# Kernel tuning notes

Hardware: AMD Instinct MI355X
Metric: run time of the kernel (lower is better)

The kernel has to match this reference:

```python
import jax, jax.numpy as jnp
import numpy as np

HEADS = 4
HEAD_DIM = 32  # hidden_dim // num_heads = 128 // 4
HIDDEN = 128
NEG_SLOPE = 0.2  # GATConv default


def gat_conv(x, src, dst, W, att_src, att_dst, bias):
    """PyG GATConv (concat=True, default negative_slope=0.2), eval mode.
    x: [N, F_in], src/dst: [E] (self-loops already included)."""
    N = x.shape[0]
    h = (x @ W).reshape(N, HEADS, HEAD_DIM)               # [N, H, D]
    a_src = jnp.einsum('nhd,hd->nh', h, att_src)          # [N, H]
    a_dst = jnp.einsum('nhd,hd->nh', h, att_dst)
    e = jax.nn.leaky_relu(a_src[src] + a_dst[dst], NEG_SLOPE)  # [E, H]
    # numerically stable softmax over incoming edges of each dst node
    m = jax.ops.segment_max(e, dst, num_segments=N)
    m = jnp.where(jnp.isfinite(m), m, 0.0)
    p = jnp.exp(e - m[dst])
    denom = jax.ops.segment_sum(p, dst, num_segments=N)
    alpha = p / (denom[dst] + 1e-16)                      # [E, H]
    out = jax.ops.segment_sum(h[src] * alpha[..., None], dst, num_segments=N)
    return out.reshape(N, HEADS * HEAD_DIM) + bias


def setup_inputs() -> dict:
    key = jax.random.key(0)
    ks = jax.random.split(key, 20)
    n_news, n_tweets, E = 20000, 80000, 1600000
    N = n_news + n_tweets
    s = 0.05
    inp = {
        'x_news': jax.random.normal(ks[0], (n_news, 768), jnp.float32),
        'x_tweets': jax.random.normal(ks[1], (n_tweets, 512), jnp.float32),
        'edge_index': jax.random.randint(ks[2], (2, E), 0, N, jnp.int32),
        'W_news': jax.random.normal(ks[3], (768, HIDDEN), jnp.float32) * s,
        'b_news': jnp.zeros((HIDDEN,), jnp.float32),
        'W_tw': jax.random.normal(ks[4], (512, HIDDEN), jnp.float32) * s,
        'b_tw': jnp.zeros((HIDDEN,), jnp.float32),
        'gat1_W': jax.random.normal(ks[5], (HIDDEN, HIDDEN), jnp.float32) * s,
        'gat1_as': jax.random.normal(ks[6], (HEADS, HEAD_DIM), jnp.float32) * s,
        'gat1_ad': jax.random.normal(ks[7], (HEADS, HEAD_DIM), jnp.float32) * s,
        'gat1_b': jnp.zeros((HIDDEN,), jnp.float32),
        'gat2_W': jax.random.normal(ks[8], (HIDDEN, HIDDEN), jnp.float32) * s,
        'gat2_as': jax.random.normal(ks[9], (HEADS, HEAD_DIM), jnp.float32) * s,
        'gat2_ad': jax.random.normal(ks[10], (HEADS, HEAD_DIM), jnp.float32) * s,
        'gat2_b': jnp.zeros((HIDDEN,), jnp.float32),
        'Wc1': jax.random.normal(ks[11], (HIDDEN, HIDDEN // 2), jnp.float32) * s,
        'bc1': jnp.zeros((HIDDEN // 2,), jnp.float32),
        'Wc2': jax.random.normal(ks[12], (HIDDEN // 2, 2), jnp.float32) * s,
        'bc2': jnp.zeros((2,), jnp.float32),
    }
    return inp


def reference(x_news, x_tweets, edge_index, W_news, b_news, W_tw, b_tw,
              gat1_W, gat1_as, gat1_ad, gat1_b,
              gat2_W, gat2_as, gat2_ad, gat2_b,
              Wc1, bc1, Wc2, bc2):
    n_news = x_news.shape[0]
    # encoders (dropout is identity in eval)
    h_news = jax.nn.relu(x_news @ W_news + b_news)
    h_tw = jax.nn.relu(x_tweets @ W_tw + b_tw)
    x = jnp.concatenate([h_news, h_tw], axis=0)           # [N, 128]
    N = x.shape[0]
    # GATConv default: add self-loops
    loops = jnp.arange(N, dtype=edge_index.dtype)
    src = jnp.concatenate([edge_index[0], loops])
    dst = jnp.concatenate([edge_index[1], loops])
    x = jax.nn.elu(gat_conv(x, src, dst, gat1_W, gat1_as, gat1_ad, gat1_b))
    x = jax.nn.elu(gat_conv(x, src, dst, gat2_W, gat2_as, gat2_ad, gat2_b))
    news_emb = x[:n_news]
    out = jax.nn.relu(news_emb @ Wc1 + bc1) @ Wc2 + bc2   # [n_news, 2]
    return out
```

## Files before the change

### kernel.cpp

```cpp
#include <hip/hip_runtime.h>
#include <hip/hip_bf16.h>
#include <type_traits>

typedef __attribute__((ext_vector_type(8))) short bf16x8;
typedef __attribute__((ext_vector_type(8))) unsigned short u16x8;
typedef __attribute__((ext_vector_type(4))) float f32x4;

__device__ __forceinline__ unsigned short f2b(float f) {
  union { float f; unsigned u; } c; c.f = f;
  return (unsigned short)((c.u + 0x7fffu + ((c.u >> 16) & 1u)) >> 16);
}
__device__ __forceinline__ float b2f(unsigned short v) {
  return __uint_as_float((unsigned)v << 16);
}

constexpr int BK = 64;
constexpr int LS = BK + 8;

template<int BM, int K, int ACT, int LOGITS, typename AT>
__device__ __forceinline__ void gemm_body(
    int bid, unsigned short* As,
    const AT* __restrict__ A, int M,
    const unsigned short* __restrict__ WT, const float* __restrict__ bias,
    unsigned short* __restrict__ C,
    const float* __restrict__ att_src, const float* __restrict__ att_dst,
    float* __restrict__ a_src, float* __restrict__ a_dst)
{
  constexpr int WTM = BM;
  constexpr int WTN = 32;
  constexpr int MF = WTM / 16;
  constexpr int NF = WTN / 16;
  constexpr int HPW = 1;
  const int t = threadIdx.x;
  const int lane = t & 63;
  const int wc = t >> 6;
  const long row0 = (long)bid * BM;

  f32x4 acc[MF][NF] = {};

  for (int k0 = 0; k0 < K; k0 += BK) {
    if constexpr (std::is_same<AT, float>::value) {
#pragma unroll
      for (int i = 0; i < BM / 16; ++i) {
        int idx = t + i * 256;
        int r = idx >> 4;
        int kq = idx & 15;
        long gr = row0 + r; if (gr >= M) gr = M - 1;
        const float4 v = *(const float4*)(A + gr * K + k0 + kq * 4);
        ushort4 b;
        b.x = f2b(v.x); b.y = f2b(v.y); b.z = f2b(v.z); b.w = f2b(v.w);
        *(ushort4*)(&As[r * LS + kq * 4]) = b;
      }
    } else {
#pragma unroll
      for (int i = 0; i < BM / 32; ++i) {
        int idx = t + i * 256;
        int r = idx >> 3;
        int k8 = idx & 7;
        long gr = row0 + r; if (gr >= M) gr = M - 1;
        u16x8 v = *(const u16x8*)(A + gr * K + k0 + k8 * 8);
        *(u16x8*)(&As[r * LS + k8 * 8]) = v;
      }
    }
    __syncthreads();
#pragma unroll
    for (int kk = 0; kk < BK; kk += 32) {
      const int koff = kk + (lane >> 4) * 8;
      bf16x8 af[MF], bfr[NF];
#pragma unroll
      for (int n = 0; n < NF; ++n)
        bfr[n] = *(const bf16x8*)(WT + (long)(wc * WTN + n * 16 + (lane & 15)) * K + k0 + koff);
#pragma unroll
      for (int m = 0; m < MF; ++m)
        af[m] = *(const bf16x8*)(&As[(m * 16 + (lane & 15)) * LS + koff]);
#pragma unroll
      for (int m = 0; m < MF; ++m)
#pragma unroll
        for (int n = 0; n < NF; ++n)
          acc[m][n] = __builtin_amdgcn_mfma_f32_16x16x32_bf16(af[m], bfr[n], acc[m][n], 0, 0, 0);
    }
    __syncthreads();
  }

  float asv[NF], adv[NF];
  if (LOGITS) {
#pragma unroll
    for (int n = 0; n < NF; ++n) {
      int dim = n * 16 + (lane & 15);
      asv[n] = att_src[wc * 32 + dim];
      adv[n] = att_dst[wc * 32 + dim];
    }
  }

#pragma unroll
  for (int m = 0; m < MF; ++m) {
#pragma unroll
    for (int j = 0; j < 4; ++j) {
      long gr = row0 + m * 16 + (lane >> 4) * 4 + j;
      if (gr < M) {
#pragma unroll
        for (int n = 0; n < NF; ++n) {
          int c = wc * WTN + n * 16 + (lane & 15);
          float v = acc[m][n][j];
          if (bias) v += bias[c];
          if (ACT == 1) v = fmaxf(v, 0.f);
          C[gr * 128 + c] = f2b(v);
        }
      }
      if (LOGITS) {
        float sa = fmaf(acc[m][0][j], asv[0], acc[m][1][j] * asv[1]);
        float da = fmaf(acc[m][0][j], adv[0], acc[m][1][j] * adv[1]);
#pragma unroll
        for (int off = 1; off < 16; off <<= 1) {
          sa += __shfl_xor(sa, off);
          da += __shfl_xor(da, off);
        }
        if ((lane & 15) == 0 && gr < M) {
          a_src[gr * 4 + wc] = sa;
          a_dst[gr * 4 + wc] = da;
        }
      }
    }
  }
}

__device__ __forceinline__ void hist_body(int bid, int* cnt, const int* __restrict__ dst,
                                          int E, int* __restrict__ bcount, int nb)
{
  int t = threadIdx.x;
  for (int b = t; b < 512; b += 256) cnt[b] = 0;
  __syncthreads();
  int e0 = bid * 8192;
  for (int i = 0; i < 32; ++i) {
    int e = e0 + i * 256 + t;
    if (e < E) atomicAdd(&cnt[dst[e] >> 8], 1);
  }
  __syncthreads();
  for (int b = t; b < nb; b += 256) {
    int c = cnt[b];
    if (c > 0) atomicAdd(&bcount[b], c);
  }
}

__device__ __forceinline__ void scatter_body(int bid, int* s, const int* __restrict__ src,
                                             const int* __restrict__ dst, int E,
                                             int* __restrict__ bcur, int2* __restrict__ pairs)
{
  int* cnt = s;
  int* base = s + 512;
  int* rcur = s + 1024;
  int t = threadIdx.x;
  for (int b = t; b < 512; b += 256) { cnt[b] = 0; rcur[b] = 0; }
  __syncthreads();
  int e0 = bid * 8192;
  for (int i = 0; i < 32; ++i) {
    int e = e0 + i * 256 + t;
    if (e < E) atomicAdd(&cnt[dst[e] >> 8], 1);
  }
  __syncthreads();
  for (int b = t; b < 512; b += 256) {
    int c = cnt[b];
    if (c > 0) base[b] = atomicAdd(&bcur[b], c);
  }
  __syncthreads();
  for (int i = 0; i < 32; ++i) {
    int e = e0 + i * 256 + t;
    if (e < E) {
      int d = dst[e];
      int b = d >> 8;
      int off = atomicAdd(&rcur[b], 1);
      int2 p; p.x = src[e]; p.y = d;
      pairs[base[b] + off] = p;
    }
  }
}

__global__ __launch_bounds__(256) void mega1_kernel(
    int nb_tw, int nb_news,
    const float* __restrict__ x_tw, int n_tw, const unsigned short* __restrict__ WT_tw,
    const float* __restrict__ b_tw, unsigned short* __restrict__ out_tw,
    const float* __restrict__ x_news, int n_news, const unsigned short* __restrict__ WT_news,
    const float* __restrict__ b_news, unsigned short* __restrict__ out_news,
    const int* __restrict__ dst, int E, int* __restrict__ bcount, int nb)
{
  __shared__ unsigned short sh[64 * LS];
  int bid = blockIdx.x;
  if (bid < nb_tw) {
    gemm_body<64, 512, 1, 0, float>(bid, sh, x_tw, n_tw, WT_tw, b_tw, out_tw,
                                    nullptr, nullptr, nullptr, nullptr);
  } else if (bid < nb_tw + nb_news) {
    gemm_body<32, 768, 1, 0, float>(bid - nb_tw, sh, x_news, n_news, WT_news,
                                    b_news, out_news, nullptr, nullptr, nullptr, nullptr);
  } else {
    hist_body(bid - nb_tw - nb_news, (int*)sh, dst, E, bcount, nb);
  }
}

__global__ __launch_bounds__(256) void mega3_kernel(
    int nb_gemm,
    const unsigned short* __restrict__ x_feat, int N, const unsigned short* __restrict__ WT_g1,
    unsigned short* __restrict__ h_feat,
    const float* __restrict__ g1as, const float* __restrict__ g1ad,
    float* __restrict__ a_src, float* __restrict__ a_dst,
    const int* __restrict__ src, const int* __restrict__ dst, int E,
    int* __restrict__ bcur, int2* __restrict__ pairs)
{
  __shared__ unsigned short sh[64 * LS];
  int bid = blockIdx.x;
  if (bid < nb_gemm) {
    gemm_body<64, 128, 0, 1, unsigned short>(bid, sh, x_feat, N, WT_g1, nullptr,
                                             h_feat, g1as, g1ad, a_src, a_dst);
  } else {
    scatter_body(bid - nb_gemm, (int*)sh, src, dst, E, bcur, pairs);
  }
}

template<int BM, int K, int ACT, int LOGITS, typename AT>
__global__ __launch_bounds__(256) void gemm_kernel(
    const AT* __restrict__ A, int M,
    const unsigned short* __restrict__ WT, const float* __restrict__ bias,
    unsigned short* __restrict__ C,
    const float* __restrict__ att_src, const float* __restrict__ att_dst,
    float* __restrict__ a_src, float* __restrict__ a_dst)
{
  __shared__ unsigned short sh[BM * LS];
  gemm_body<BM, K, ACT, LOGITS, AT>(blockIdx.x, sh, A, M, WT, bias, C,
                                    att_src, att_dst, a_src, a_dst);
}

__global__ void transpose_all_kernel(const float* __restrict__ W0, unsigned short* __restrict__ T0,
                                     const float* __restrict__ W1, unsigned short* __restrict__ T1,
                                     const float* __restrict__ W2, unsigned short* __restrict__ T2,
                                     const float* __restrict__ W3, unsigned short* __restrict__ T3)
{
  int r = blockIdx.x * 256 + threadIdx.x;
  if (r < 128 * 768) { int c = r / 768, k = r - c * 768; T0[r] = f2b(W0[(size_t)k * 128 + c]); return; }
  r -= 128 * 768;
  if (r < 128 * 512) { int c = r / 512, k = r - c * 512; T1[r] = f2b(W1[(size_t)k * 128 + c]); return; }
  r -= 128 * 512;
  if (r < 128 * 128) { T2[r] = f2b(W2[(size_t)(r & 127) * 128 + (r >> 7)]); return; }
  r -= 128 * 128;
  if (r < 128 * 128) { T3[r] = f2b(W3[(size_t)(r & 127) * 128 + (r >> 7)]); return; }
}

__global__ __launch_bounds__(512) void bucket_scan_kernel(const int* __restrict__ bcount, int nb, int E,
                                                          int* __restrict__ bstart, int* __restrict__ bcur,
                                                          int* __restrict__ row_ptr, int N)
{
  __shared__ int s[512];
  int t = threadIdx.x;
  int my = (t < nb) ? bcount[t] : 0;
  s[t] = my;
  __syncthreads();
  for (int off = 1; off < 512; off <<= 1) {
    int v = (t >= off) ? s[t - off] : 0;
    __syncthreads();
    s[t] += v;
    __syncthreads();
  }
  int excl = s[t] - my;
  if (t < nb) { bstart[t] = excl; bcur[t] = excl; }
  if (t == 0) { bstart[nb] = E; row_ptr[N] = E; }
}

__global__ __launch_bounds__(256) void bucket_csr_kernel(const int2* __restrict__ pairs,
                                                         const int* __restrict__ bstart, int N,
                                                         int* __restrict__ row_ptr, int* __restrict__ col_idx)
{
  __shared__ int cnt[256];
  __shared__ int excl[256];
  __shared__ int cur[256];
  int t = threadIdx.x;
  int nodebase = blockIdx.x << 8;
  int start = bstart[blockIdx.x];
  int size = bstart[blockIdx.x + 1] - start;
  cnt[t] = 0;
  __syncthreads();
  for (int i = t; i < size; i += 256)
    atomicAdd(&cnt[pairs[start + i].y & 255], 1);
  __syncthreads();
  int my = cnt[t];
  excl[t] = my;
  __syncthreads();
  for (int off = 1; off < 256; off <<= 1) {
    int v = (t >= off) ? excl[t - off] : 0;
    __syncthreads();
    excl[t] += v;
    __syncthreads();
  }
  int ex = excl[t] - my;
  if (nodebase + t < N) row_ptr[nodebase + t] = start + ex;
  excl[t] = ex;
  cur[t] = 0;
  __syncthreads();
  for (int i = t; i < size; i += 256) {
    int2 p = pairs[start + i];
    int local = p.y & 255;
    int pos = start + excl[local] + atomicAdd(&cur[local], 1);
    col_idx[pos] = p.x;
  }
}

__global__ void gat_aggregate_kernel(const unsigned short* __restrict__ h, const float* __restrict__ a_src,
                                     const float* __restrict__ a_dst, const int* __restrict__ row_ptr,
                                     const int* __restrict__ col_idx, const float* __restrict__ bias,
                                     int N, unsigned short* __restrict__ out)
{
  int n = (blockIdx.x * blockDim.x + threadIdx.x) >> 6;
  int lane = threadIdx.x & 63;
  if (n >= N) return;
  const int sub = lane >> 4;
  const int sl = lane & 15;
  const int head = sl >> 2;
  const int beg = row_ptr[n], end = row_ptr[n + 1];
  const float adst = a_dst[(size_t)n * 4 + head];

  float slf = a_src[(size_t)n * 4 + head] + adst;
  slf = fmaxf(slf, 0.2f * slf);
  float ps = (sub == 0) ? __expf(slf) : 0.f;
  float denom = ps;
  float acc[8];
  {
    const u16x8 hs = *(const u16x8*)(h + (size_t)n * 128 + 8 * sl);
#pragma unroll
    for (int j = 0; j < 8; ++j) acc[j] = ps * b2f(hs[j]);
  }

  int e = beg + sub;
  for (; e + 4 < end; e += 8) {
    const int s0 = col_idx[e];
    const int s1 = col_idx[e + 4];
    const u16x8 h0 = *(const u16x8*)(h + (size_t)s0 * 128 + 8 * sl);
    const u16x8 h1 = *(const u16x8*)(h + (size_t)s1 * 128 + 8 * sl);
    float l0 = a_src[(size_t)s0 * 4 + head] + adst;
    float l1 = a_src[(size_t)s1 * 4 + head] + adst;
    l0 = fmaxf(l0, 0.2f * l0);
    l1 = fmaxf(l1, 0.2f * l1);
    const float p0 = __expf(l0);
    const float p1 = __expf(l1);
    denom += p0 + p1;
#pragma unroll
    for (int j = 0; j < 8; ++j) {
      acc[j] = fmaf(p0, b2f(h0[j]), acc[j]);
      acc[j] = fmaf(p1, b2f(h1[j]), acc[j]);
    }
  }
  if (e < end) {
    const int s = col_idx[e];
    const u16x8 hv = *(const u16x8*)(h + (size_t)s * 128 + 8 * sl);
    float lg = a_src[(size_t)s * 4 + head] + adst;
    lg = fmaxf(lg, 0.2f * lg);
    const float p = __expf(lg);
    denom += p;
#pragma unroll
    for (int j = 0; j < 8; ++j) acc[j] = fmaf(p, b2f(hv[j]), acc[j]);
  }

#pragma unroll
  for (int j = 0; j < 8; ++j) {
    acc[j] += __shfl_xor(acc[j], 16);
    acc[j] += __shfl_xor(acc[j], 32);
  }
  denom += __shfl_xor(denom, 16);
  denom += __shfl_xor(denom, 32);

  if (sub == 0) {
    const float inv = 1.0f / (denom + 1e-16f);
    const float4 b0 = *(const float4*)(bias + 8 * sl);
    const float4 b1 = *(const float4*)(bias + 8 * sl + 4);
    float o[8];
    o[0] = acc[0] * inv + b0.x; o[1] = acc[1] * inv + b0.y;
    o[2] = acc[2] * inv + b0.z; o[3] = acc[3] * inv + b0.w;
    o[4] = acc[4] * inv + b1.x; o[5] = acc[5] * inv + b1.y;
    o[6] = acc[6] * inv + b1.z; o[7] = acc[7] * inv + b1.w;
    u16x8 r;
#pragma unroll
    for (int j = 0; j < 8; ++j) {
      float v = (o[j] > 0.f) ? o[j] : expm1f(o[j]);
      r[j] = f2b(v);
    }
    *(u16x8*)(out + (size_t)n * 128 + 8 * sl) = r;
  }
}

__global__ void classifier_kernel(const unsigned short* __restrict__ x, const float* __restrict__ Wc1,
                                  const float* __restrict__ bc1, const float* __restrict__ Wc2,
                                  const float* __restrict__ bc2, float* __restrict__ out, int M)
{
  int row = (blockIdx.x * blockDim.x + threadIdx.x) >> 6;
  int lane = threadIdx.x & 63;
  if (row >= M) return;
  const unsigned short* xr = x + (size_t)row * 128;
  float c = 0.f;
#pragma unroll 8
  for (int k = 0; k < 128; k += 2) {
    unsigned v = *(const unsigned*)(xr + k);
    c = fmaf(__uint_as_float(v << 16), Wc1[k * 64 + lane], c);
    c = fmaf(__uint_as_float(v & 0xffff0000u), Wc1[(k + 1) * 64 + lane], c);
  }
  c += bc1[lane];
  c = fmaxf(c, 0.f);
  float o0 = c * Wc2[lane * 2 + 0];
  float o1 = c * Wc2[lane * 2 + 1];
#pragma unroll
  for (int off = 1; off < 64; off <<= 1) {
    o0 += __shfl_xor(o0, off);
    o1 += __shfl_xor(o1, off);
  }
  if (lane == 0) {
    out[(size_t)row * 2 + 0] = o0 + bc2[0];
    out[(size_t)row * 2 + 1] = o1 + bc2[1];
  }
}

extern "C" void kernel_launch(void* const* d_in, const int* in_sizes, int n_in,
                              void* d_out, int out_size, void* d_ws, size_t ws_size,
                              hipStream_t stream)
{
  const float* x_news = (const float*)d_in[0];
  const float* x_tw   = (const float*)d_in[1];
  const int*   ei     = (const int*)d_in[2];
  const float* W_news = (const float*)d_in[3];
  const float* b_news = (const float*)d_in[4];
  const float* W_tw   = (const float*)d_in[5];
  const float* b_tw   = (const float*)d_in[6];
  const float* g1W  = (const float*)d_in[7];
  const float* g1as = (const float*)d_in[8];
  const float* g1ad = (const float*)d_in[9];
  const float* g1b  = (const float*)d_in[10];
  const float* g2W  = (const float*)d_in[11];
  const float* g2as = (const float*)d_in[12];
  const float* g2ad = (const float*)d_in[13];
  const float* g2b  = (const float*)d_in[14];
  const float* Wc1  = (const float*)d_in[15];
  const float* bc1  = (const float*)d_in[16];
  const float* Wc2  = (const float*)d_in[17];
  const float* bc2  = (const float*)d_in[18];

  const int n_news = in_sizes[0] / 768;
  const int n_tw   = in_sizes[1] / 512;
  const int N = n_news + n_tw;
  const int E = in_sizes[2] / 2;
  const int* src = ei;
  const int* dst = ei + E;
  const int nb = (N + 255) >> 8;

  char* ws = (char*)d_ws;
  size_t off = 0;
  auto alloc = [&](size_t bytes) -> void* {
    void* p = ws + off;
    off += (bytes + 255) & ~(size_t)255;
    return p;
  };
  unsigned short* x_feat = (unsigned short*)alloc((size_t)N * 128 * 2);
  unsigned short* h_feat = (unsigned short*)alloc((size_t)N * 128 * 2);
  float* a_src   = (float*)alloc((size_t)N * 4 * 4);
  float* a_dst   = (float*)alloc((size_t)N * 4 * 4);
  int*   row_ptr = (int*)alloc((size_t)(N + 1) * 4);
  int*   col_idx = (int*)alloc((size_t)E * 4);
  int2*  pairs   = (int2*)alloc((size_t)E * 8);
  int*   bcount  = (int*)alloc(2048);
  int*   bstart  = (int*)alloc(2052);
  int*   bcur    = (int*)alloc(2048);
  unsigned short* WT_news = (unsigned short*)alloc((size_t)128 * 768 * 2);
  unsigned short* WT_tw   = (unsigned short*)alloc((size_t)128 * 512 * 2);
  unsigned short* WT_g1   = (unsigned short*)alloc((size_t)128 * 128 * 2);
  unsigned short* WT_g2   = (unsigned short*)alloc((size_t)128 * 128 * 2);

  hipMemsetAsync(bcount, 0, 2048, stream);

  transpose_all_kernel<<<768, 256, 0, stream>>>(W_news, WT_news, W_tw, WT_tw, g1W, WT_g1, g2W, WT_g2);

  const int nb_tw = (n_tw + 63) / 64;
  const int nb_news = (n_news + 31) / 32;
  const int nb_hist = (E + 8191) / 8192;
  mega1_kernel<<<nb_tw + nb_news + nb_hist, 256, 0, stream>>>(
      nb_tw, nb_news,
      x_tw, n_tw, WT_tw, b_tw, x_feat + (size_t)n_news * 128,
      x_news, n_news, WT_news, b_news, x_feat,
      dst, E, bcount, nb);

  bucket_scan_kernel<<<1, 512, 0, stream>>>(bcount, nb, E, bstart, bcur, row_ptr, N);

  const int nb_g = (N + 63) / 64;
  mega3_kernel<<<nb_g + nb_hist, 256, 0, stream>>>(
      nb_g, x_feat, N, WT_g1, h_feat, g1as, g1ad, a_src, a_dst,
      src, dst, E, bcur, pairs);

  bucket_csr_kernel<<<nb, 256, 0, stream>>>(pairs, bstart, N, row_ptr, col_idx);

  gat_aggregate_kernel<<<(N + 3) / 4, 256, 0, stream>>>(h_feat, a_src, a_dst, row_ptr, col_idx, g1b, N, x_feat);

  gemm_kernel<64, 128, 0, 1, unsigned short><<<nb_g, 256, 0, stream>>>(
      x_feat, N, WT_g2, nullptr, h_feat, g2as, g2ad, a_src, a_dst);
  gat_aggregate_kernel<<<(N + 3) / 4, 256, 0, stream>>>(h_feat, a_src, a_dst, row_ptr, col_idx, g2b, N, x_feat);

  classifier_kernel<<<(n_news + 3) / 4, 256, 0, stream>>>(x_feat, Wc1, bc1, Wc2, bc2, (float*)d_out, n_news);
}
```

Measured before the change: 375.0 us.

## Double-buffer GEMM A tiles in LDS with register prefetch of next K slice

The GEMM body now loads the next K slice of A into registers while MFMAs run on the current LDS buffer, then writes it to a second LDS buffer, removing one barrier per iteration. The goal is to hide global load latency behind compute in the encoder and GAT projection GEMMs. It doubles the LDS footprint and adds register pressure, which can reduce occupancy. It also grows LDS for the fused histogram and scatter blocks that share the same kernels.

Measured after the change: 378.3 us. No clear change (+0.9%).

```diff
diff --git a/kernel.cpp b/kernel.cpp
--- a/kernel.cpp
+++ b/kernel.cpp
@@ -26,43 +26,67 @@
     const float* __restrict__ att_src, const float* __restrict__ att_dst,
     float* __restrict__ a_src, float* __restrict__ a_dst)
 {
-  constexpr int WTM = BM;
+  constexpr bool F32 = std::is_same<AT, float>::value;
   constexpr int WTN = 32;
-  constexpr int MF = WTM / 16;
-  constexpr int NF = WTN / 16;
-  constexpr int HPW = 1;
+  constexpr int MF = BM / 16;
+  constexpr int NF = 2;
+  constexpr int NLD = F32 ? (BM / 16) : (BM / 32);
   const int t = threadIdx.x;
   const int lane = t & 63;
   const int wc = t >> 6;
   const long row0 = (long)bid * BM;
 
   f32x4 acc[MF][NF] = {};
-
-  for (int k0 = 0; k0 < K; k0 += BK) {
-    if constexpr (std::is_same<AT, float>::value) {
-#pragma unroll
-      for (int i = 0; i < BM / 16; ++i) {
+  float4 rF[F32 ? NLD : 1];
+  u16x8  rB[F32 ? 1 : NLD];
+
+  auto issue_loads = [&](int k0) {
+    if constexpr (F32) {
+#pragma unroll
+      for (int i = 0; i < NLD; ++i) {
         int idx = t + i * 256;
-        int r = idx >> 4;
-        int kq = idx & 15;
+        int r = idx >> 4, kq = idx & 15;
         long gr = row0 + r; if (gr >= M) gr = M - 1;
-        const float4 v = *(const float4*)(A + gr * K + k0 + kq * 4);
-        ushort4 b;
-        b.x = f2b(v.x); b.y = f2b(v.y); b.z = f2b(v.z); b.w = f2b(v.w);
-        *(ushort4*)(&As[r * LS + kq * 4]) = b;
+        rF[i] = *(const float4*)(A + gr * K + k0 + kq * 4);
       }
     } else {
 #pragma unroll
-      for (int i = 0; i < BM / 32; ++i) {
+      for (int i = 0; i < NLD; ++i) {
         int idx = t + i * 256;
-        int r = idx >> 3;
-        int k8 = idx & 7;
+        int r = idx >> 3, k8 = idx & 7;
         long gr = row0 + r; if (gr >= M) gr = M - 1;
-        u16x8 v = *(const u16x8*)(A + gr * K + k0 + k8 * 8);
-        *(u16x8*)(&As[r * LS + k8 * 8]) = v;
+        rB[i] = *(const u16x8*)(A + gr * K + k0 + k8 * 8);
       }
     }
+  };
+  auto write_lds = [&](unsigned short* buf) {
+    if constexpr (F32) {
+#pragma unroll
+      for (int i = 0; i < NLD; ++i) {
+        int idx = t + i * 256;
+        int r = idx >> 4, kq = idx & 15;
+        ushort4 b;
+        b.x = f2b(rF[i].x); b.y = f2b(rF[i].y); b.z = f2b(rF[i].z); b.w = f2b(rF[i].w);
+        *(ushort4*)(&buf[r * LS + kq * 4]) = b;
+      }
+    } else {
+#pragma unroll
+      for (int i = 0; i < NLD; ++i) {
+        int idx = t + i * 256;
+        int r = idx >> 3, k8 = idx & 7;
+        *(u16x8*)(&buf[r * LS + k8 * 8]) = rB[i];
+      }
+    }
+  };
+
+  issue_loads(0);
+  write_lds(As);
+  int cur = 0;
+
+  for (int k0 = 0; k0 < K; k0 += BK) {
     __syncthreads();
+    if (k0 + BK < K) issue_loads(k0 + BK);
+    unsigned short* buf = As + cur * BM * LS;
 #pragma unroll
     for (int kk = 0; kk < BK; kk += 32) {
       const int koff = kk + (lane >> 4) * 8;
@@ -72,14 +96,14 @@
         bfr[n] = *(const bf16x8*)(WT + (long)(wc * WTN + n * 16 + (lane & 15)) * K + k0 + koff);
 #pragma unroll
       for (int m = 0; m < MF; ++m)
-        af[m] = *(const bf16x8*)(&As[(m * 16 + (lane & 15)) * LS + koff]);
+        af[m] = *(const bf16x8*)(&buf[(m * 16 + (lane & 15)) * LS + koff]);
 #pragma unroll
       for (int m = 0; m < MF; ++m)
 #pragma unroll
         for (int n = 0; n < NF; ++n)
           acc[m][n] = __builtin_amdgcn_mfma_f32_16x16x32_bf16(af[m], bfr[n], acc[m][n], 0, 0, 0);
     }
-    __syncthreads();
+    if (k0 + BK < K) { write_lds(As + (cur ^ 1) * BM * LS); cur ^= 1; }
   }
 
   float asv[NF], adv[NF];
@@ -183,7 +207,7 @@
     const float* __restrict__ b_news, unsigned short* __restrict__ out_news,
     const int* __restrict__ dst, int E, int* __restrict__ bcount, int nb)
 {
-  __shared__ unsigned short sh[64 * LS];
+  __shared__ unsigned short sh[2 * 64 * LS];
   int bid = blockIdx.x;
   if (bid < nb_tw) {
     gemm_body<64, 512, 1, 0, float>(bid, sh, x_tw, n_tw, WT_tw, b_tw, out_tw,
@@ -205,7 +229,7 @@
     const int* __restrict__ src, const int* __restrict__ dst, int E,
     int* __restrict__ bcur, int2* __restrict__ pairs)
 {
-  __shared__ unsigned short sh[64 * LS];
+  __shared__ unsigned short sh[2 * 64 * LS];
   int bid = blockIdx.x;
   if (bid < nb_gemm) {
     gemm_body<64, 128, 0, 1, unsigned short>(bid, sh, x_feat, N, WT_g1, nullptr,
@@ -223,7 +247,7 @@
     const float* __restrict__ att_src, const float* __restrict__ att_dst,
     float* __restrict__ a_src, float* __restrict__ a_dst)
 {
-  __shared__ unsigned short sh[BM * LS];
+  __shared__ unsigned short sh[2 * BM * LS];
   gemm_body<BM, K, ACT, LOGITS, AT>(blockIdx.x, sh, A, M, WT, bias, C,
                                     att_src, att_dst, a_src, a_dst);
 }
```

## Restructure GEMM so each wave owns 16 rows across all 128 columns

Applied to the files above, without the earlier changes.

The GEMM body drops the shared-memory A tile and its __syncthreads. Each wave now loads its own 16-row A fragment directly from global memory, converting fp32 to bf16 in registers, and computes all 8 column fragments (128 outputs). The logits epilogue is reworked so each wave computes all four head dot-products at once. The news encoder block size changes from 32 to 64 rows to match. This removes LDS traffic and barriers, but every wave now re-reads the full weight matrix from global or L2, and accumulator register usage grows.

After: 515.6 us. 1.38x slower.

```diff
diff --git a/kernel.cpp b/kernel.cpp
--- a/kernel.cpp
+++ b/kernel.cpp
@@ -14,110 +14,90 @@
   return __uint_as_float((unsigned)v << 16);
 }
 
-constexpr int BK = 64;
-constexpr int LS = BK + 8;
-
 template<int BM, int K, int ACT, int LOGITS, typename AT>
 __device__ __forceinline__ void gemm_body(
-    int bid, unsigned short* As,
+    int bid,
     const AT* __restrict__ A, int M,
     const unsigned short* __restrict__ WT, const float* __restrict__ bias,
     unsigned short* __restrict__ C,
     const float* __restrict__ att_src, const float* __restrict__ att_dst,
     float* __restrict__ a_src, float* __restrict__ a_dst)
 {
-  constexpr int WTM = BM;
-  constexpr int WTN = 32;
-  constexpr int MF = WTM / 16;
-  constexpr int NF = WTN / 16;
-  constexpr int HPW = 1;
+  constexpr bool F32 = std::is_same<AT, float>::value;
   const int t = threadIdx.x;
   const int lane = t & 63;
-  const int wc = t >> 6;
-  const long row0 = (long)bid * BM;
-
-  f32x4 acc[MF][NF] = {};
-
-  for (int k0 = 0; k0 < K; k0 += BK) {
-    if constexpr (std::is_same<AT, float>::value) {
-#pragma unroll
-      for (int i = 0; i < BM / 16; ++i) {
-        int idx = t + i * 256;
-        int r = idx >> 4;
-        int kq = idx & 15;
-        long gr = row0 + r; if (gr >= M) gr = M - 1;
-        const float4 v = *(const float4*)(A + gr * K + k0 + kq * 4);
-        ushort4 b;
-        b.x = f2b(v.x); b.y = f2b(v.y); b.z = f2b(v.z); b.w = f2b(v.w);
-        *(ushort4*)(&As[r * LS + kq * 4]) = b;
+  const int wv = t >> 6;
+  const int fr = lane & 15;
+  const int kb = lane >> 4;
+  const long row0 = (long)bid * BM + wv * 16;
+  long arow = row0 + fr; if (arow >= M) arow = M - 1;
+  const AT* aptr = A + arow * K + kb * 8;
+  const unsigned short* bptr = WT + (long)fr * K + kb * 8;
+
+  f32x4 acc[8] = {};
+
+#pragma unroll 2
+  for (int k0 = 0; k0 < K; k0 += 32) {
+    bf16x8 af;
+    if constexpr (F32) {
+      const float4 v0 = *(const float4*)(aptr + k0);
+      const float4 v1 = *(const float4*)(aptr + k0 + 4);
+      union { u16x8 u; bf16x8 b; } cv;
+      cv.u[0] = f2b(v0.x); cv.u[1] = f2b(v0.y); cv.u[2] = f2b(v0.z); cv.u[3] = f2b(v0.w);
+      cv.u[4] = f2b(v1.x); cv.u[5] = f2b(v1.y); cv.u[6] = f2b(v1.z); cv.u[7] = f2b(v1.w);
+      af = cv.b;
+    } else {
+      af = *(const bf16x8*)(aptr + k0);
+    }
+#pragma unroll
+    for (int n = 0; n < 8; ++n) {
+      const bf16x8 bf = *(const bf16x8*)(bptr + (long)n * 16 * K + k0);
+      acc[n] = __builtin_amdgcn_mfma_f32_16x16x32_bf16(af, bf, acc[n], 0, 0, 0);
+    }
+  }
+
+  float asv[8], adv[8];
+  if (LOGITS) {
+#pragma unroll
+    for (int n = 0; n < 8; ++n) {
+      asv[n] = att_src[n * 16 + fr];
+      adv[n] = att_dst[n * 16 + fr];
+    }
+  }
+
+#pragma unroll
+  for (int j = 0; j < 4; ++j) {
+    long gr = row0 + kb * 4 + j;
+    if (gr < M) {
+#pragma unroll
+      for (int n = 0; n < 8; ++n) {
+        int c = n * 16 + fr;
+        float v = acc[n][j];
+        if (bias) v += bias[c];
+        if (ACT == 1) v = fmaxf(v, 0.f);
+        C[gr * 128 + c] = f2b(v);
       }
-    } else {
-#pragma unroll
-      for (int i = 0; i < BM / 32; ++i) {
-        int idx = t + i * 256;
-        int r = idx >> 3;
-        int k8 = idx & 7;
-        long gr = row0 + r; if (gr >= M) gr = M - 1;
-        u16x8 v = *(const u16x8*)(A + gr * K + k0 + k8 * 8);
-        *(u16x8*)(&As[r * LS + k8 * 8]) = v;
+    }
+    if (LOGITS) {
+      float sa[4], da[4];
+#pragma unroll
+      for (int g = 0; g < 4; ++g) {
+        sa[g] = fmaf(acc[2 * g][j], asv[2 * g], acc[2 * g + 1][j] * asv[2 * g + 1]);
+        da[g] = fmaf(acc[2 * g][j], adv[2 * g], acc[2 * g + 1][j] * adv[2 * g + 1]);
       }
-    }
-    __syncthreads();
-#pragma unroll
-    for (int kk = 0; kk < BK; kk += 32) {
-      const int koff = kk + (lane >> 4) * 8;
-      bf16x8 af[MF], bfr[NF];
-#pragma unroll
-      for (int n = 0; n < NF; ++n)
-        bfr[n] = *(const bf16x8*)(WT + (long)(wc * WTN + n * 16 + (lane & 15)) * K + k0 + koff);
-#pragma unroll
-      for (int m = 0; m < MF; ++m)
-        af[m] = *(const bf16x8*)(&As[(m * 16 + (lane & 15)) * LS + koff]);
-#pragma unroll
-      for (int m = 0; m < MF; ++m)
-#pragma unroll
-        for (int n = 0; n < NF; ++n)
-          acc[m][n] = __builtin_amdgcn_mfma_f32_16x16x32_bf16(af[m], bfr[n], acc[m][n], 0, 0, 0);
-    }
-    __syncthreads();
-  }
-
-  float asv[NF], adv[NF];
-  if (LOGITS) {
-#pragma unroll
-    for (int n = 0; n < NF; ++n) {
-      int dim = n * 16 + (lane & 15);
-      asv[n] = att_src[wc * 32 + dim];
-      adv[n] = att_dst[wc * 32 + dim];
-    }
-  }
-
-#pragma unroll
-  for (int m = 0; m < MF; ++m) {
-#pragma unroll
-    for (int j = 0; j < 4; ++j) {
-      long gr = row0 + m * 16 + (lane >> 4) * 4 + j;
-      if (gr < M) {
-#pragma unroll
-        for (int n = 0; n < NF; ++n) {
-          int c = wc * WTN + n * 16 + (lane & 15);
-          float v = acc[m][n][j];
-          if (bias) v += bias[c];
-          if (ACT == 1) v = fmaxf(v, 0.f);
-          C[gr * 128 + c] = f2b(v);
+#pragma unroll
+      for (int off = 1; off < 16; off <<= 1) {
+#pragma unroll
+        for (int g = 0; g < 4; ++g) {
+          sa[g] += __shfl_xor(sa[g], off);
+          da[g] += __shfl_xor(da[g], off);
         }
       }
-      if (LOGITS) {
-        float sa = fmaf(acc[m][0][j], asv[0], acc[m][1][j] * asv[1]);
-        float da = fmaf(acc[m][0][j], adv[0], acc[m][1][j] * adv[1]);
-#pragma unroll
-        for (int off = 1; off < 16; off <<= 1) {
-          sa += __shfl_xor(sa, off);
-          da += __shfl_xor(da, off);
-        }
-        if ((lane & 15) == 0 && gr < M) {
-          a_src[gr * 4 + wc] = sa;
-          a_dst[gr * 4 + wc] = da;
+      if (fr == 0 && gr < M) {
+#pragma unroll
+        for (int g = 0; g < 4; ++g) {
+          a_src[gr * 4 + g] = sa[g];
+          a_dst[gr * 4 + g] = da[g];
         }
       }
     }
@@ -183,16 +163,16 @@
     const float* __restrict__ b_news, unsigned short* __restrict__ out_news,
     const int* __restrict__ dst, int E, int* __restrict__ bcount, int nb)
 {
-  __shared__ unsigned short sh[64 * LS];
+  __shared__ int shi[512];
   int bid = blockIdx.x;
   if (bid < nb_tw) {
-    gemm_body<64, 512, 1, 0, float>(bid, sh, x_tw, n_tw, WT_tw, b_tw, out_tw,
+    gemm_body<64, 512, 1, 0, float>(bid, x_tw, n_tw, WT_tw, b_tw, out_tw,
                                     nullptr, nullptr, nullptr, nullptr);
   } else if (bid < nb_tw + nb_news) {
-    gemm_body<32, 768, 1, 0, float>(bid - nb_tw, sh, x_news, n_news, WT_news,
+    gemm_body<64, 768, 1, 0, float>(bid - nb_tw, x_news, n_news, WT_news,
                                     b_news, out_news, nullptr, nullptr, nullptr, nullptr);
   } else {
-    hist_body(bid - nb_tw - nb_news, (int*)sh, dst, E, bcount, nb);
+    hist_body(bid - nb_tw - nb_news, shi, dst, E, bcount, nb);
   }
 }
 
@@ -205,13 +185,13 @@
     const int* __restrict__ src, const int* __restrict__ dst, int E,
     int* __restrict__ bcur, int2* __restrict__ pairs)
 {
-  __shared__ unsigned short sh[64 * LS];
+  __shared__ int shi[1536];
   int bid = blockIdx.x;
   if (bid < nb_gemm) {
-    gemm_body<64, 128, 0, 1, unsigned short>(bid, sh, x_feat, N, WT_g1, nullptr,
+    gemm_body<64, 128, 0, 1, unsigned short>(bid, x_feat, N, WT_g1, nullptr,
                                              h_feat, g1as, g1ad, a_src, a_dst);
   } else {
-    scatter_body(bid - nb_gemm, (int*)sh, src, dst, E, bcur, pairs);
+    scatter_body(bid - nb_gemm, shi, src, dst, E, bcur, pairs);
   }
 }
 
@@ -223,8 +203,7 @@
     const float* __restrict__ att_src, const float* __restrict__ att_dst,
     float* __restrict__ a_src, float* __restrict__ a_dst)
 {
-  __shared__ unsigned short sh[BM * LS];
-  gemm_body<BM, K, ACT, LOGITS, AT>(blockIdx.x, sh, A, M, WT, bias, C,
+  gemm_body<BM, K, ACT, LOGITS, AT>(blockIdx.x, A, M, WT, bias, C,
                                     att_src, att_dst, a_src, a_dst);
 }
 
@@ -472,7 +451,7 @@
   transpose_all_kernel<<<768, 256, 0, stream>>>(W_news, WT_news, W_tw, WT_tw, g1W, WT_g1, g2W, WT_g2);
 
   const int nb_tw = (n_tw + 63) / 64;
-  const int nb_news = (n_news + 31) / 32;
+  const int nb_news = (n_news + 63) / 64;
   const int nb_hist = (E + 8191) / 8192;
   mega1_kernel<<<nb_tw + nb_news + nb_hist, 256, 0, stream>>>(
       nb_tw, nb_news,
```

## Stage weight tiles in shared memory and limit second-layer aggregation to news nodes

Applied to the files above, without the earlier changes.

The GEMM body now cooperatively loads the 128-column weight tile for each K-step into shared memory, so warps stop reading B fragments directly from global memory. The shared buffer grows to hold both A and B tiles, which may reduce occupancy. Separately, the second GAT aggregation runs only over the first n_news destination nodes, because the classifier reads only news embeddings. This skips about 80% of that aggregation's work while keeping the output the same.

Result: faster. 309.4 us (-17.5%).

```diff
diff --git a/kernel.cpp b/kernel.cpp
--- a/kernel.cpp
+++ b/kernel.cpp
@@ -19,18 +19,16 @@
 
 template<int BM, int K, int ACT, int LOGITS, typename AT>
 __device__ __forceinline__ void gemm_body(
-    int bid, unsigned short* As,
+    int bid, unsigned short* As, unsigned short* Bs,
     const AT* __restrict__ A, int M,
     const unsigned short* __restrict__ WT, const float* __restrict__ bias,
     unsigned short* __restrict__ C,
     const float* __restrict__ att_src, const float* __restrict__ att_dst,
     float* __restrict__ a_src, float* __restrict__ a_dst)
 {
-  constexpr int WTM = BM;
   constexpr int WTN = 32;
-  constexpr int MF = WTM / 16;
-  constexpr int NF = WTN / 16;
-  constexpr int HPW = 1;
+  constexpr int MF = BM / 16;
+  constexpr int NF = 2;
   const int t = threadIdx.x;
   const int lane = t & 63;
   const int wc = t >> 6;
@@ -62,6 +60,14 @@
         *(u16x8*)(&As[r * LS + k8 * 8]) = v;
       }
     }
+#pragma unroll
+    for (int i = 0; i < 4; ++i) {
+      int idx = t + i * 256;
+      int col = idx >> 3;
+      int k8 = idx & 7;
+      u16x8 v = *(const u16x8*)(WT + (long)col * K + k0 + k8 * 8);
+      *(u16x8*)(&Bs[col * LS + k8 * 8]) = v;
+    }
     __syncthreads();
 #pragma unroll
     for (int kk = 0; kk < BK; kk += 32) {
@@ -69,7 +75,7 @@
       bf16x8 af[MF], bfr[NF];
 #pragma unroll
       for (int n = 0; n < NF; ++n)
-        bfr[n] = *(const bf16x8*)(WT + (long)(wc * WTN + n * 16 + (lane & 15)) * K + k0 + koff);
+        bfr[n] = *(const bf16x8*)(&Bs[(wc * WTN + n * 16 + (lane & 15)) * LS + koff]);
 #pragma unroll
       for (int m = 0; m < MF; ++m)
         af[m] = *(const bf16x8*)(&As[(m * 16 + (lane & 15)) * LS + koff]);
@@ -183,13 +189,13 @@
     const float* __restrict__ b_news, unsigned short* __restrict__ out_news,
     const int* __restrict__ dst, int E, int* __restrict__ bcount, int nb)
 {
-  __shared__ unsigned short sh[64 * LS];
+  __shared__ unsigned short sh[(64 + 128) * LS];
   int bid = blockIdx.x;
   if (bid < nb_tw) {
-    gemm_body<64, 512, 1, 0, float>(bid, sh, x_tw, n_tw, WT_tw, b_tw, out_tw,
+    gemm_body<64, 512, 1, 0, float>(bid, sh, sh + 64 * LS, x_tw, n_tw, WT_tw, b_tw, out_tw,
                                     nullptr, nullptr, nullptr, nullptr);
   } else if (bid < nb_tw + nb_news) {
-    gemm_body<32, 768, 1, 0, float>(bid - nb_tw, sh, x_news, n_news, WT_news,
+    gemm_body<32, 768, 1, 0, float>(bid - nb_tw, sh, sh + 32 * LS, x_news, n_news, WT_news,
                                     b_news, out_news, nullptr, nullptr, nullptr, nullptr);
   } else {
     hist_body(bid - nb_tw - nb_news, (int*)sh, dst, E, bcount, nb);
@@ -205,10 +211,10 @@
     const int* __restrict__ src, const int* __restrict__ dst, int E,
     int* __restrict__ bcur, int2* __restrict__ pairs)
 {
-  __shared__ unsigned short sh[64 * LS];
+  __shared__ unsigned short sh[(64 + 128) * LS];
   int bid = blockIdx.x;
   if (bid < nb_gemm) {
-    gemm_body<64, 128, 0, 1, unsigned short>(bid, sh, x_feat, N, WT_g1, nullptr,
+    gemm_body<64, 128, 0, 1, unsigned short>(bid, sh, sh + 64 * LS, x_feat, N, WT_g1, nullptr,
                                              h_feat, g1as, g1ad, a_src, a_dst);
   } else {
     scatter_body(bid - nb_gemm, (int*)sh, src, dst, E, bcur, pairs);
@@ -223,8 +229,8 @@
     const float* __restrict__ att_src, const float* __restrict__ att_dst,
     float* __restrict__ a_src, float* __restrict__ a_dst)
 {
-  __shared__ unsigned short sh[BM * LS];
-  gemm_body<BM, K, ACT, LOGITS, AT>(blockIdx.x, sh, A, M, WT, bias, C,
+  __shared__ unsigned short sh[(BM + 128) * LS];
+  gemm_body<BM, K, ACT, LOGITS, AT>(blockIdx.x, sh, sh + BM * LS, A, M, WT, bias, C,
                                     att_src, att_dst, a_src, a_dst);
 }
 
@@ -304,11 +310,11 @@
 __global__ void gat_aggregate_kernel(const unsigned short* __restrict__ h, const float* __restrict__ a_src,
                                      const float* __restrict__ a_dst, const int* __restrict__ row_ptr,
                                      const int* __restrict__ col_idx, const float* __restrict__ bias,
-                                     int N, unsigned short* __restrict__ out)
+                                     int Nproc, unsigned short* __restrict__ out)
 {
   int n = (blockIdx.x * blockDim.x + threadIdx.x) >> 6;
   int lane = threadIdx.x & 63;
-  if (n >= N) return;
+  if (n >= Nproc) return;
   const int sub = lane >> 4;
   const int sl = lane & 15;
   const int head = sl >> 2;
@@ -483,7 +489,8 @@
   bucket_scan_kernel<<<1, 512, 0, stream>>>(bcount, nb, E, bstart, bcur, row_ptr, N);
 
   const int nb_g = (N + 63) / 64;
-  mega3_kernel<<<nb_g + nb_hist, 256, 0, stream>>>(
+  const int nb_hist2 = (E + 8191) / 8192;
+  mega3_kernel<<<nb_g + nb_hist2, 256, 0, stream>>>(
       nb_g, x_feat, N, WT_g1, h_feat, g1as, g1ad, a_src, a_dst,
       src, dst, E, bcur, pairs);
 
@@ -493,7 +500,7 @@
 
   gemm_kernel<64, 128, 0, 1, unsigned short><<<nb_g, 256, 0, stream>>>(
       x_feat, N, WT_g2, nullptr, h_feat, g2as, g2ad, a_src, a_dst);
-  gat_aggregate_kernel<<<(N + 3) / 4, 256, 0, stream>>>(h_feat, a_src, a_dst, row_ptr, col_idx, g2b, N, x_feat);
+  gat_aggregate_kernel<<<(n_news + 3) / 4, 256, 0, stream>>>(h_feat, a_src, a_dst, row_ptr, col_idx, g2b, n_news, x_feat);
 
   classifier_kernel<<<(n_news + 3) / 4, 256, 0, stream>>>(x_feat, Wc1, bc1, Wc2, bc2, (float*)d_out, n_news);
 }
```
